# Optimization experiments

Measured on AMD Instinct MI355X. Metric: run time of the kernel, lower is better.

## Reference

```python
import jax, jax.numpy as jnp
import numpy as np
from jax import lax

B, L = 2, 5000            # images, candidate lines per image
C_IN, C_LOI = 256, 128    # backbone channels, dim_loi
H = W = 256               # feature-map spatial size (indices clamped to 255)
N_PTS0, N_PTS1 = 32, 8    # points sampled per line, after maxpool
POOL = N_PTS0 // N_PTS1   # MaxPool1d kernel/stride = 4
PLANES = C_LOI // 2       # Bottleneck1D mid channels
EPS = 1e-5


def setup_inputs() -> dict:
    key = jax.random.key(0)
    ks = jax.random.split(key, 16)
    f32 = jnp.float32
    s = 0.05
    feature = jax.random.normal(ks[0], (B, C_IN, H, W), f32)
    lines = jax.random.uniform(ks[1], (B, L, 2, 2), f32, minval=0.0, maxval=255.0)
    return {
        "feature": feature,
        "lines": lines,
        "fc1_w": jax.random.normal(ks[2], (C_LOI, C_IN), f32) * s,
        "fc1_b": jnp.zeros((C_LOI,), f32),
        "bn1_g": jnp.ones((C_LOI,), f32),
        "bn1_b": jnp.zeros((C_LOI,), f32),
        "bn1_m": jax.random.normal(ks[3], (C_LOI,), f32) * 0.1,
        "bn1_v": jax.random.uniform(ks[4], (C_LOI,), f32, minval=0.5, maxval=1.5),
        "conv1_w": jax.random.normal(ks[5], (PLANES, C_LOI), f32) * s,
        "conv1_b": jnp.zeros((PLANES,), f32),
        "bn2_g": jnp.ones((PLANES,), f32),
        "bn2_b": jnp.zeros((PLANES,), f32),
        "bn2_m": jax.random.normal(ks[6], (PLANES,), f32) * 0.1,
        "bn2_v": jax.random.uniform(ks[7], (PLANES,), f32, minval=0.5, maxval=1.5),
        "conv2_w": jax.random.normal(ks[8], (PLANES, PLANES, 3), f32) * s,
        "conv2_b": jnp.zeros((PLANES,), f32),
        "bn3_g": jnp.ones((PLANES,), f32),
        "bn3_b": jnp.zeros((PLANES,), f32),
        "bn3_m": jax.random.normal(ks[9], (PLANES,), f32) * 0.1,
        "bn3_v": jax.random.uniform(ks[10], (PLANES,), f32, minval=0.5, maxval=1.5),
        "conv3_w": jax.random.normal(ks[11], (C_LOI, PLANES), f32) * s,
        "conv3_b": jnp.zeros((C_LOI,), f32),
        "fc2_w": jax.random.normal(ks[12], (3, C_LOI * N_PTS1), f32) * s,
        "fc2_b": jnp.zeros((3,), f32),
    }


def _bn(x, g, b, m, v):
    # eval-mode BatchNorm1d over [N, C, T]
    inv = g / jnp.sqrt(v + EPS)
    return x * inv[None, :, None] + (b - m * inv)[None, :, None]


def _bilinear_sample(feat, lines):
    # feat: [B, C, H, W], lines: [B, L, 2, 2] -> [B, L, C, N_PTS0]
    lam = jnp.linspace(0.0, 1.0, N_PTS0, dtype=feat.dtype)[:, None]  # [P,1]
    # p = lam * endpoint0 + (1-lam) * endpoint1 - 0.5  -> [B, L, P, 2]
    p = lines[:, :, 0:1, :] * lam + lines[:, :, 1:2, :] * (1.0 - lam) - 0.5
    px, py = p[..., 0], p[..., 1]                       # [B, L, P]
    px0 = jnp.clip(jnp.floor(px), 0.0, 255.0)
    py0 = jnp.clip(jnp.floor(py), 0.0, 255.0)
    px1 = jnp.clip(px0 + 1.0, 0.0, 255.0)
    py1 = jnp.clip(py0 + 1.0, 0.0, 255.0)
    ix0, iy0 = px0.astype(jnp.int32), py0.astype(jnp.int32)
    ix1, iy1 = px1.astype(jnp.int32), py1.astype(jnp.int32)
    w00 = (px1 - px) * (py1 - py)
    w10 = (px - px0) * (py1 - py)
    w01 = (px1 - px) * (py - py0)
    w11 = (px - px0) * (py - py0)

    def one_image(f, a0, b0, a1, b1, c00, c10, c01, c11):
        # f: [C,H,W], indices/weights: [L,P] -> [C,L,P]
        return (f[:, a0, b0] * c00 + f[:, a1, b0] * c10 +
                f[:, a0, b1] * c01 + f[:, a1, b1] * c11)

    xp = jax.vmap(one_image)(feat, ix0, iy0, ix1, iy1, w00, w10, w01, w11)
    return jnp.transpose(xp, (0, 2, 1, 3))  # [B, L, C, P]


def _forward(feature, lines, fc1_w, fc1_b, bn1_g, bn1_b, bn1_m, bn1_v,
             conv1_w, conv1_b, bn2_g, bn2_b, bn2_m, bn2_v,
             conv2_w, conv2_b, bn3_g, bn3_b, bn3_m, bn3_v,
             conv3_w, conv3_b, fc2_w, fc2_b):
    # fc1: 1x1 conv over the backbone feature map
    x = jnp.einsum('oc,bchw->bohw', fc1_w, feature) + fc1_b[None, :, None, None]
    xp = _bilinear_sample(x, lines)                     # [B, L, C_LOI, P]
    xp = xp.reshape(B * L, C_LOI, N_PTS0)
    # MaxPool1d(kernel=POOL, stride=POOL)
    xp = xp.reshape(B * L, C_LOI, N_PTS1, POOL).max(axis=-1)  # [N, C, T]
    # Bottleneck1D residual branch: BN-ReLU-Conv1(k1)-BN-ReLU-Conv(k3)-BN-ReLU-Conv(k1)
    h = jax.nn.relu(_bn(xp, bn1_g, bn1_b, bn1_m, bn1_v))
    h = jnp.einsum('oc,nct->not', conv1_w, h) + conv1_b[None, :, None]
    h = jax.nn.relu(_bn(h, bn2_g, bn2_b, bn2_m, bn2_v))
    h = lax.conv_general_dilated(h, conv2_w, window_strides=(1,),
                                 padding=((1, 1),),
                                 dimension_numbers=('NCH', 'OIH', 'NCH'))
    h = h + conv2_b[None, :, None]
    h = jax.nn.relu(_bn(h, bn3_g, bn3_b, bn3_m, bn3_v))
    h = jnp.einsum('oc,nct->not', conv3_w, h) + conv3_b[None, :, None]
    xp = xp + h
    # fc2: ReLU + Linear(dim_loi * n_pts1 -> 3)
    flat = jax.nn.relu(xp).reshape(B * L, C_LOI * N_PTS1)
    return flat @ fc2_w.T + fc2_b


def reference(feature, lines, fc1_w, fc1_b, bn1_g, bn1_b, bn1_m, bn1_v,
              conv1_w, conv1_b, bn2_g, bn2_b, bn2_m, bn2_v,
              conv2_w, conv2_b, bn3_g, bn3_b, bn3_m, bn3_v,
              conv3_w, conv3_b, fc2_w, fc2_b):
    return _forward(feature, lines, fc1_w, fc1_b, bn1_g, bn1_b, bn1_m, bn1_v,
                    conv1_w, conv1_b, bn2_g, bn2_b, bn2_m, bn2_v,
                    conv2_w, conv2_b, bn3_g, bn3_b, bn3_m, bn3_v,
                    conv3_w, conv3_b, fc2_w, fc2_b)
```

## Files before the change

kernel.cpp:

```cpp
#include <hip/hip_runtime.h>
#include <hip/hip_bf16.h>

#define BB 2
#define LL 5000
#define CIN 256
#define CLOI 128
#define HH 256
#define WW 256
#define HWP (HH*WW)
#define NPTS0 32
#define NPTS1 8
#define PLANES 64
#define EPSV 1e-5f

#define X_BYTES   ((size_t)BB * HWP * CLOI * 2)
#define XS_BYTES  ((size_t)BB * LL * 1024 * 2)
#define W1S_OFF   (X_BYTES + XS_BYTES)
#define W2S_OFF   (W1S_OFF + 16384)
#define W3S_OFF   (W2S_OFF + 24576)
#define B1P_OFF   (W3S_OFF + 16384)
#define B2P_OFF   (B1P_OFF + 256)
#define S1_OFF    (B2P_OFF + 256)
#define T1_OFF    (S1_OFF + 512)
#define W0S_OFF   (T1_OFF + 512)

typedef unsigned int uint;
typedef unsigned short ushort;
typedef __attribute__((ext_vector_type(8))) short short8;
typedef __attribute__((ext_vector_type(4))) float f32x4;

__device__ __forceinline__ float bf2f(ushort u) {
    uint v = ((uint)u) << 16;
    return __uint_as_float(v);
}
__device__ __forceinline__ ushort f2bf(float f) {
    uint x = __float_as_uint(f);
    uint r = (x + 0x7fffu + ((x >> 16) & 1u)) >> 16;
    return (ushort)r;
}
__device__ __forceinline__ uint pack2(float a, float b) {
    return (uint)f2bf(a) | ((uint)f2bf(b) << 16);
}

__global__ __launch_bounds__(256) void fc1_kernel(
    const float* __restrict__ feature, const ushort* __restrict__ w0s,
    const float* __restrict__ fc1_b, ushort* __restrict__ xout)
{
    __shared__ ushort sF[32 * 64 * 8];

    int tid = threadIdx.x;
    int tile = blockIdx.x;
    int b = tile >> 10;
    int p0 = (tile & 1023) << 6;
    int wv = tid >> 6, lane = tid & 63;
    int q = lane >> 4, ln = lane & 15;

    short8 afr[8][2];
#pragma unroll
    for (int kg = 0; kg < 8; kg++)
#pragma unroll
        for (int mt = 0; mt < 2; mt++)
            afr[kg][mt] = *(const short8*)(w0s + ((size_t)((kg * 4 + q) * 128 + wv * 32 + mt * 16 + ln)) * 8);

    const float* fb = feature + (size_t)b * CIN * HWP + p0;
    int g_ = tid >> 4;
    int qd = tid & 15;
#pragma unroll
    for (int s = 0; s < 2; s++) {
        int g = s * 16 + g_;
        const float* src = fb + (size_t)(g * 8) * HWP + qd * 4;
        float4 rv[8];
#pragma unroll
        for (int j = 0; j < 8; j++) rv[j] = *(const float4*)(src + (size_t)j * HWP);
#pragma unroll
        for (int i = 0; i < 4; i++) {
            uint4 u;
            u.x = pack2(((const float*)&rv[0])[i], ((const float*)&rv[1])[i]);
            u.y = pack2(((const float*)&rv[2])[i], ((const float*)&rv[3])[i]);
            u.z = pack2(((const float*)&rv[4])[i], ((const float*)&rv[5])[i]);
            u.w = pack2(((const float*)&rv[6])[i], ((const float*)&rv[7])[i]);
            *(uint4*)(&sF[(g * 64 + qd * 4 + i) * 8]) = u;
        }
    }
    __syncthreads();

    const f32x4 fzero = { 0.f, 0.f, 0.f, 0.f };
    f32x4 acc[2][4];
#pragma unroll
    for (int mt = 0; mt < 2; mt++)
#pragma unroll
        for (int nt = 0; nt < 4; nt++) acc[mt][nt] = fzero;

#pragma unroll
    for (int kg = 0; kg < 8; kg++) {
#pragma unroll
        for (int nt = 0; nt < 4; nt++) {
            short8 bfr = *(short8*)(&sF[((kg * 4 + q) * 64 + nt * 16 + ln) * 8]);
            acc[0][nt] = __builtin_amdgcn_mfma_f32_16x16x32_bf16(afr[kg][0], bfr, acc[0][nt], 0, 0, 0);
            acc[1][nt] = __builtin_amdgcn_mfma_f32_16x16x32_bf16(afr[kg][1], bfr, acc[1][nt], 0, 0, 0);
        }
    }

    float bias[8];
    *(float4*)bias       = *(const float4*)(fc1_b + wv * 32 + q * 4);
    *(float4*)(bias + 4) = *(const float4*)(fc1_b + wv * 32 + 16 + q * 4);
    ushort* xrow = xout + (size_t)b * HWP * CLOI;
#pragma unroll
    for (int mt = 0; mt < 2; mt++)
#pragma unroll
        for (int nt = 0; nt < 4; nt++) {
            uint2 u;
            u.x = pack2(acc[mt][nt][0] + bias[mt * 4 + 0], acc[mt][nt][1] + bias[mt * 4 + 1]);
            u.y = pack2(acc[mt][nt][2] + bias[mt * 4 + 2], acc[mt][nt][3] + bias[mt * 4 + 3]);
            *(uint2*)(xrow + (size_t)(p0 + nt * 16 + ln) * CLOI + wv * 32 + mt * 16 + q * 4) = u;
        }
}

__global__ __launch_bounds__(256) void prep_kernel(
    const float* __restrict__ conv1_w, const float* __restrict__ conv1_b,
    const float* __restrict__ bn2_g, const float* __restrict__ bn2_b,
    const float* __restrict__ bn2_m, const float* __restrict__ bn2_v,
    const float* __restrict__ conv2_w, const float* __restrict__ conv2_b,
    const float* __restrict__ bn3_g, const float* __restrict__ bn3_b,
    const float* __restrict__ bn3_m, const float* __restrict__ bn3_v,
    const float* __restrict__ conv3_w,
    const float* __restrict__ bn1_g, const float* __restrict__ bn1_b,
    const float* __restrict__ bn1_m, const float* __restrict__ bn1_v,
    const float* __restrict__ fc1_w,
    ushort* __restrict__ w1s, ushort* __restrict__ w2s, ushort* __restrict__ w3s,
    float* __restrict__ b1p, float* __restrict__ b2p,
    float* __restrict__ s1o, float* __restrict__ t1o,
    ushort* __restrict__ w0s)
{
    int idx = blockIdx.x * 256 + threadIdx.x;
    if (idx < 8192) {
        int kg = idx >> 9, rem = idx & 511, m = rem >> 3, j = rem & 7;
        int c = kg * 8 + j;
        float s2 = bn2_g[m] * rsqrtf(bn2_v[m] + EPSV);
        w1s[idx] = f2bf(conv1_w[m * 128 + c] * s2);
    }
    if (idx < 12288) {
        int dt = idx >> 12, rem = idx & 4095;
        int kg = rem >> 9, m = (rem >> 3) & 63, j = rem & 7;
        int i = kg * 8 + j;
        float s3 = bn3_g[m] * rsqrtf(bn3_v[m] + EPSV);
        w2s[idx] = f2bf(conv2_w[m * 192 + i * 3 + dt] * s3);
    }
    if (idx < 8192) {
        int kg = idx >> 10, rem = idx & 1023, m = rem >> 3, j = rem & 7;
        w3s[idx] = f2bf(conv3_w[m * 64 + kg * 8 + j]);
    }
    if (idx < 32768) {
        int grp = idx >> 10, rem = idx & 1023, m = rem >> 3, j = rem & 7;
        w0s[idx] = f2bf(fc1_w[m * CIN + grp * 8 + j]);
    }
    if (idx < 64) {
        float s2 = bn2_g[idx] * rsqrtf(bn2_v[idx] + EPSV);
        b1p[idx] = conv1_b[idx] * s2 + bn2_b[idx] - bn2_m[idx] * s2;
        float s3 = bn3_g[idx] * rsqrtf(bn3_v[idx] + EPSV);
        b2p[idx] = conv2_b[idx] * s3 + bn3_b[idx] - bn3_m[idx] * s3;
    }
    if (idx < 128) {
        float s1 = bn1_g[idx] * rsqrtf(bn1_v[idx] + EPSV);
        s1o[idx] = s1;
        t1o[idx] = bn1_b[idx] - bn1_m[idx] * s1;
    }
}

__global__ __launch_bounds__(256, 3) void sample_head_kernel(
    const ushort* __restrict__ x, const float* __restrict__ lines,
    const ushort* __restrict__ w1s, const ushort* __restrict__ w2s,
    const ushort* __restrict__ w3s,
    const float* __restrict__ b1p, const float* __restrict__ b2p,
    const float* __restrict__ s1g, const float* __restrict__ t1g,
    const float* __restrict__ conv3_b,
    const float* __restrict__ fc2_w, const float* __restrict__ fc2_b,
    float* __restrict__ out)
{
    __shared__ ushort sXS[8192];
    __shared__ ushort sH1[8192];
    __shared__ ushort sB2[4096];
    __shared__ int   sIdx[8][32][4];
    __shared__ float sWt[8][32][4];
    __shared__ float sB1[64], sB2b[64], sB3b[128];

    int tid = threadIdx.x;
    int wv = tid >> 6, lane = tid & 63;
    int q = lane >> 4, ln = lane & 15;
    int L0 = blockIdx.x * 8;
    int b = L0 / LL;
    int colg = wv * 16 + ln;

    if (tid < 128) sB3b[tid] = conv3_b[tid];
    if (tid < 64)  { sB1[tid] = b1p[tid]; sB2b[tid] = b2p[tid]; }

    float s1a = s1g[2 * lane], s1c = s1g[2 * lane + 1];
    float t1a = t1g[2 * lane], t1c = t1g[2 * lane + 1];

    {
        int l = tid >> 5, j = tid & 31;
        float lam = (float)j * (1.0f / 31.0f);
        const float* lp = lines + (size_t)(L0 + l) * 4;
        float e0x = lp[0], e0y = lp[1], e1x = lp[2], e1y = lp[3];
        float px = e0x * lam + e1x * (1.f - lam) - 0.5f;
        float py = e0y * lam + e1y * (1.f - lam) - 0.5f;
        float px0 = fminf(fmaxf(floorf(px), 0.f), 255.f);
        float py0 = fminf(fmaxf(floorf(py), 0.f), 255.f);
        float px1 = fminf(px0 + 1.f, 255.f);
        float py1 = fminf(py0 + 1.f, 255.f);
        int ix0 = (int)px0, iy0 = (int)py0, ix1 = (int)px1, iy1 = (int)py1;
        sIdx[l][j][0] = ix0 * WW + iy0;
        sIdx[l][j][1] = ix1 * WW + iy0;
        sIdx[l][j][2] = ix0 * WW + iy1;
        sIdx[l][j][3] = ix1 * WW + iy1;
        sWt[l][j][0] = (px1 - px) * (py1 - py);
        sWt[l][j][1] = (px - px0) * (py1 - py);
        sWt[l][j][2] = (px1 - px) * (py - py0);
        sWt[l][j][3] = (px - px0) * (py - py0);
    }
    __syncthreads();

    const uint* xb = (const uint*)(x + (size_t)b * HWP * CLOI);
    int kg = lane >> 2;
    int j2 = (lane & 3) * 2;
    int swz = (kg & 7) << 3;

    for (int l = 0; l < 8; l++) {
        float m00 = -INFINITY, m10 = -INFINITY;
        float m01 = -INFINITY, m11 = -INFINITY;
#pragma unroll
        for (int jj = 0; jj < 8; jj++) {
            int j = wv * 8 + jj;
            int i00 = sIdx[l][j][0], i10 = sIdx[l][j][1], i01 = sIdx[l][j][2], i11 = sIdx[l][j][3];
            float w00 = sWt[l][j][0], w10 = sWt[l][j][1], w01 = sWt[l][j][2], w11 = sWt[l][j][3];
            uint u00 = xb[(size_t)i00 * 64 + lane];
            uint u10 = xb[(size_t)i10 * 64 + lane];
            uint u01 = xb[(size_t)i01 * 64 + lane];
            uint u11 = xb[(size_t)i11 * 64 + lane];
            float v0 = bf2f((ushort)(u00 & 0xffff)) * w00 + bf2f((ushort)(u10 & 0xffff)) * w10
                     + bf2f((ushort)(u01 & 0xffff)) * w01 + bf2f((ushort)(u11 & 0xffff)) * w11;
            float v1 = bf2f((ushort)(u00 >> 16)) * w00 + bf2f((ushort)(u10 >> 16)) * w10
                     + bf2f((ushort)(u01 >> 16)) * w01 + bf2f((ushort)(u11 >> 16)) * w11;
            if (jj < 4) { m00 = fmaxf(m00, v0); m10 = fmaxf(m10, v1); }
            else        { m01 = fmaxf(m01, v0); m11 = fmaxf(m11, v1); }
        }
        int col0 = l * 8 + 2 * wv;
        int base0 = (kg * 64 + col0) * 8 + j2;
        *(uint*)(&sXS[base0 ^ swz])       = pack2(m00, m10);
        *(uint*)(&sXS[(base0 + 8) ^ swz]) = pack2(m01, m11);
        float h00 = fmaxf(m00 * s1a + t1a, 0.f), h10 = fmaxf(m10 * s1c + t1c, 0.f);
        float h01 = fmaxf(m01 * s1a + t1a, 0.f), h11 = fmaxf(m11 * s1c + t1c, 0.f);
        *(uint*)(&sH1[base0 ^ swz])       = pack2(h00, h10);
        *(uint*)(&sH1[(base0 + 8) ^ swz]) = pack2(h01, h11);
    }
    __syncthreads();

    const short8 bzero = { 0, 0, 0, 0, 0, 0, 0, 0 };
    const f32x4 fzero = { 0.f, 0.f, 0.f, 0.f };

    f32x4 acc1[4];
#pragma unroll
    for (int mt = 0; mt < 4; mt++) acc1[mt] = fzero;
#pragma unroll
    for (int ks = 0; ks < 4; ks++) {
        int kk = ks * 4 + q;
        short8 bfrag = *(short8*)(&sH1[((kk * 64 + colg) * 8) ^ ((kk & 7) << 3)]);
#pragma unroll
        for (int mt = 0; mt < 4; mt++) {
            short8 a = *(const short8*)(w1s + (kk * 64 + mt * 16 + ln) * 8);
            acc1[mt] = __builtin_amdgcn_mfma_f32_16x16x32_bf16(a, bfrag, acc1[mt], 0, 0, 0);
        }
    }
#pragma unroll
    for (int mt = 0; mt < 4; mt++) {
        int m0 = mt * 16 + q * 4;
        float v0 = fmaxf(acc1[mt][0] + sB1[m0 + 0], 0.f);
        float v1 = fmaxf(acc1[mt][1] + sB1[m0 + 1], 0.f);
        float v2 = fmaxf(acc1[mt][2] + sB1[m0 + 2], 0.f);
        float v3 = fmaxf(acc1[mt][3] + sB1[m0 + 3], 0.f);
        uint2 u; u.x = pack2(v0, v1); u.y = pack2(v2, v3);
        *(uint2*)(&sB2[((m0 >> 3) * 64 + colg) * 8 + (m0 & 7)]) = u;
    }
    __syncthreads();

    f32x4 acc2[4];
#pragma unroll
    for (int mt = 0; mt < 4; mt++) acc2[mt] = fzero;
    int tpos = colg & 7;
#pragma unroll
    for (int dt = 0; dt < 3; dt++) {
        int tsh = tpos + dt - 1;
        bool valid = ((unsigned)tsh < 8u);
        int colr = colg + dt - 1;
        colr = colr < 0 ? 0 : (colr > 63 ? 63 : colr);
#pragma unroll
        for (int ks = 0; ks < 2; ks++) {
            int kk = ks * 4 + q;
            short8 bfrag = *(short8*)(&sB2[(kk * 64 + colr) * 8]);
            bfrag = valid ? bfrag : bzero;
#pragma unroll
            for (int mt = 0; mt < 4; mt++) {
                short8 a = *(const short8*)(w2s + dt * 4096 + (kk * 64 + mt * 16 + ln) * 8);
                acc2[mt] = __builtin_amdgcn_mfma_f32_16x16x32_bf16(a, bfrag, acc2[mt], 0, 0, 0);
            }
        }
    }
#pragma unroll
    for (int mt = 0; mt < 4; mt++) {
        int m0 = mt * 16 + q * 4;
        float v0 = fmaxf(acc2[mt][0] + sB2b[m0 + 0], 0.f);
        float v1 = fmaxf(acc2[mt][1] + sB2b[m0 + 1], 0.f);
        float v2 = fmaxf(acc2[mt][2] + sB2b[m0 + 2], 0.f);
        float v3 = fmaxf(acc2[mt][3] + sB2b[m0 + 3], 0.f);
        uint2 u; u.x = pack2(v0, v1); u.y = pack2(v2, v3);
        int idx = ((m0 >> 3) * 64 + colg) * 8 + (m0 & 7);
        *(uint2*)(&sH1[idx ^ (((m0 >> 3) & 7) << 3)]) = u;
    }
    __syncthreads();

    f32x4 acc3[8];
#pragma unroll
    for (int mt = 0; mt < 8; mt++) acc3[mt] = fzero;
#pragma unroll
    for (int ks = 0; ks < 2; ks++) {
        int kk = ks * 4 + q;
        short8 bfrag = *(short8*)(&sH1[((kk * 64 + colg) * 8) ^ ((kk & 7) << 3)]);
#pragma unroll
        for (int mt = 0; mt < 8; mt++) {
            short8 a = *(const short8*)(w3s + (kk * 128 + mt * 16 + ln) * 8);
            acc3[mt] = __builtin_amdgcn_mfma_f32_16x16x32_bf16(a, bfrag, acc3[mt], 0, 0, 0);
        }
    }

    float p0 = 0.f, p1 = 0.f, p2 = 0.f;
#pragma unroll
    for (int mt = 0; mt < 8; mt++) {
#pragma unroll
        for (int r = 0; r < 4; r++) {
            int m = mt * 16 + q * 4 + r;
            int idx = ((m >> 3) * 512 + colg * 8 + (m & 7)) ^ (((m >> 3) & 7) << 3);
            float xsv = bf2f(sXS[idx]);
            float v = fmaxf(xsv + acc3[mt][r] + sB3b[m], 0.f);
            int fi = m * 8 + tpos;
            p0 += v * fc2_w[fi];
            p1 += v * fc2_w[1024 + fi];
            p2 += v * fc2_w[2048 + fi];
        }
    }
    p0 += __shfl_xor(p0, 32); p1 += __shfl_xor(p1, 32); p2 += __shfl_xor(p2, 32);
    p0 += __shfl_xor(p0, 16); p1 += __shfl_xor(p1, 16); p2 += __shfl_xor(p2, 16);
    p0 += __shfl_xor(p0, 4);  p1 += __shfl_xor(p1, 4);  p2 += __shfl_xor(p2, 4);
    p0 += __shfl_xor(p0, 2);  p1 += __shfl_xor(p1, 2);  p2 += __shfl_xor(p2, 2);
    p0 += __shfl_xor(p0, 1);  p1 += __shfl_xor(p1, 1);  p2 += __shfl_xor(p2, 1);

    if (lane == 0 || lane == 8) {
        int line = L0 + wv * 2 + (lane >> 3);
        out[(size_t)line * 3 + 0] = p0 + fc2_b[0];
        out[(size_t)line * 3 + 1] = p1 + fc2_b[1];
        out[(size_t)line * 3 + 2] = p2 + fc2_b[2];
    }
}

extern "C" void kernel_launch(void* const* d_in, const int* in_sizes, int n_in,
                              void* d_out, int out_size, void* d_ws, size_t ws_size,
                              hipStream_t stream) {
    const float* feature = (const float*)d_in[0];
    const float* lines   = (const float*)d_in[1];
    const float* fc1_w   = (const float*)d_in[2];
    const float* fc1_b   = (const float*)d_in[3];
    const float* bn1_g   = (const float*)d_in[4];
    const float* bn1_b   = (const float*)d_in[5];
    const float* bn1_m   = (const float*)d_in[6];
    const float* bn1_v   = (const float*)d_in[7];
    const float* conv1_w = (const float*)d_in[8];
    const float* conv1_b = (const float*)d_in[9];
    const float* bn2_g   = (const float*)d_in[10];
    const float* bn2_b   = (const float*)d_in[11];
    const float* bn2_m   = (const float*)d_in[12];
    const float* bn2_v   = (const float*)d_in[13];
    const float* conv2_w = (const float*)d_in[14];
    const float* conv2_b = (const float*)d_in[15];
    const float* bn3_g   = (const float*)d_in[16];
    const float* bn3_b   = (const float*)d_in[17];
    const float* bn3_m   = (const float*)d_in[18];
    const float* bn3_v   = (const float*)d_in[19];
    const float* conv3_w = (const float*)d_in[20];
    const float* conv3_b = (const float*)d_in[21];
    const float* fc2_w   = (const float*)d_in[22];
    const float* fc2_b   = (const float*)d_in[23];
    float* out = (float*)d_out;

    char* ws = (char*)d_ws;
    ushort* x_bf = (ushort*)ws;
    ushort* w1s  = (ushort*)(ws + W1S_OFF);
    ushort* w2s  = (ushort*)(ws + W2S_OFF);
    ushort* w3s  = (ushort*)(ws + W3S_OFF);
    float*  b1p  = (float*)(ws + B1P_OFF);
    float*  b2p  = (float*)(ws + B2P_OFF);
    float*  s1g  = (float*)(ws + S1_OFF);
    float*  t1g  = (float*)(ws + T1_OFF);
    ushort* w0s  = (ushort*)(ws + W0S_OFF);

    prep_kernel<<<128, 256, 0, stream>>>(
        conv1_w, conv1_b, bn2_g, bn2_b, bn2_m, bn2_v,
        conv2_w, conv2_b, bn3_g, bn3_b, bn3_m, bn3_v,
        conv3_w, bn1_g, bn1_b, bn1_m, bn1_v, fc1_w,
        w1s, w2s, w3s, b1p, b2p, s1g, t1g, w0s);
    fc1_kernel<<<2048, 256, 0, stream>>>(feature, w0s, fc1_b, x_bf);
    sample_head_kernel<<<BB * LL / 8, 256, 0, stream>>>(
        x_bf, lines, w1s, w2s, w3s, b1p, b2p, s1g, t1g, conv3_b, fc2_w, fc2_b, out);
}
```

Measured before the change: 291.8 us.

## Drop sXS shared buffer, keep residual in registers, raise occupancy to 4 blocks

Removes the 16KB sXS shared-memory buffer by holding the pooled residual values in registers (xsu) and later writing them into sH1 once sH1 is free. The conv2 B-fragments are preloaded into registers so sB2 can be reused for the conv2 output. Launch bounds go from 3 to 4 blocks per CU. Index and weight loads from shared memory become int4/float4 vector loads. The aim is less LDS use per block for higher occupancy, which helps hide the latency of the gather-heavy sampling. The cost is more register pressure under a tighter register cap, with a risk of spilling.

```diff
diff --git a/kernel.cpp b/kernel.cpp
--- a/kernel.cpp
+++ b/kernel.cpp
@@ -167,7 +167,7 @@
     }
 }
 
-__global__ __launch_bounds__(256, 3) void sample_head_kernel(
+__global__ __launch_bounds__(256, 4) void sample_head_kernel(
     const ushort* __restrict__ x, const float* __restrict__ lines,
     const ushort* __restrict__ w1s, const ushort* __restrict__ w2s,
     const ushort* __restrict__ w3s,
@@ -177,7 +177,6 @@
     const float* __restrict__ fc2_w, const float* __restrict__ fc2_b,
     float* __restrict__ out)
 {
-    __shared__ ushort sXS[8192];
     __shared__ ushort sH1[8192];
     __shared__ ushort sB2[4096];
     __shared__ int   sIdx[8][32][4];
@@ -225,29 +224,31 @@
     int j2 = (lane & 3) * 2;
     int swz = (kg & 7) << 3;
 
+    uint xsu[8][2];
+#pragma unroll
     for (int l = 0; l < 8; l++) {
         float m00 = -INFINITY, m10 = -INFINITY;
         float m01 = -INFINITY, m11 = -INFINITY;
 #pragma unroll
         for (int jj = 0; jj < 8; jj++) {
             int j = wv * 8 + jj;
-            int i00 = sIdx[l][j][0], i10 = sIdx[l][j][1], i01 = sIdx[l][j][2], i11 = sIdx[l][j][3];
-            float w00 = sWt[l][j][0], w10 = sWt[l][j][1], w01 = sWt[l][j][2], w11 = sWt[l][j][3];
-            uint u00 = xb[(size_t)i00 * 64 + lane];
-            uint u10 = xb[(size_t)i10 * 64 + lane];
-            uint u01 = xb[(size_t)i01 * 64 + lane];
-            uint u11 = xb[(size_t)i11 * 64 + lane];
-            float v0 = bf2f((ushort)(u00 & 0xffff)) * w00 + bf2f((ushort)(u10 & 0xffff)) * w10
-                     + bf2f((ushort)(u01 & 0xffff)) * w01 + bf2f((ushort)(u11 & 0xffff)) * w11;
-            float v1 = bf2f((ushort)(u00 >> 16)) * w00 + bf2f((ushort)(u10 >> 16)) * w10
-                     + bf2f((ushort)(u01 >> 16)) * w01 + bf2f((ushort)(u11 >> 16)) * w11;
+            int4   iv = *(const int4*)(&sIdx[l][j][0]);
+            float4 wvv = *(const float4*)(&sWt[l][j][0]);
+            uint u00 = xb[(size_t)iv.x * 64 + lane];
+            uint u10 = xb[(size_t)iv.y * 64 + lane];
+            uint u01 = xb[(size_t)iv.z * 64 + lane];
+            uint u11 = xb[(size_t)iv.w * 64 + lane];
+            float v0 = bf2f((ushort)(u00 & 0xffff)) * wvv.x + bf2f((ushort)(u10 & 0xffff)) * wvv.y
+                     + bf2f((ushort)(u01 & 0xffff)) * wvv.z + bf2f((ushort)(u11 & 0xffff)) * wvv.w;
+            float v1 = bf2f((ushort)(u00 >> 16)) * wvv.x + bf2f((ushort)(u10 >> 16)) * wvv.y
+                     + bf2f((ushort)(u01 >> 16)) * wvv.z + bf2f((ushort)(u11 >> 16)) * wvv.w;
             if (jj < 4) { m00 = fmaxf(m00, v0); m10 = fmaxf(m10, v1); }
             else        { m01 = fmaxf(m01, v0); m11 = fmaxf(m11, v1); }
         }
+        xsu[l][0] = pack2(m00, m10);
+        xsu[l][1] = pack2(m01, m11);
         int col0 = l * 8 + 2 * wv;
         int base0 = (kg * 64 + col0) * 8 + j2;
-        *(uint*)(&sXS[base0 ^ swz])       = pack2(m00, m10);
-        *(uint*)(&sXS[(base0 + 8) ^ swz]) = pack2(m01, m11);
         float h00 = fmaxf(m00 * s1a + t1a, 0.f), h10 = fmaxf(m10 * s1c + t1c, 0.f);
         float h01 = fmaxf(m01 * s1a + t1a, 0.f), h11 = fmaxf(m11 * s1c + t1c, 0.f);
         *(uint*)(&sH1[base0 ^ swz])       = pack2(h00, h10);
@@ -283,10 +284,16 @@
     }
     __syncthreads();
 
-    f32x4 acc2[4];
-#pragma unroll
-    for (int mt = 0; mt < 4; mt++) acc2[mt] = fzero;
+#pragma unroll
+    for (int l = 0; l < 8; l++) {
+        int col0 = l * 8 + 2 * wv;
+        int base0 = (kg * 64 + col0) * 8 + j2;
+        *(uint*)(&sH1[base0 ^ swz])       = xsu[l][0];
+        *(uint*)(&sH1[(base0 + 8) ^ swz]) = xsu[l][1];
+    }
+
     int tpos = colg & 7;
+    short8 bfr2[3][2];
 #pragma unroll
     for (int dt = 0; dt < 3; dt++) {
         int tsh = tpos + dt - 1;
@@ -295,16 +302,26 @@
         colr = colr < 0 ? 0 : (colr > 63 ? 63 : colr);
 #pragma unroll
         for (int ks = 0; ks < 2; ks++) {
+            short8 bfrag = *(short8*)(&sB2[((ks * 4 + q) * 64 + colr) * 8]);
+            bfr2[dt][ks] = valid ? bfrag : bzero;
+        }
+    }
+    __syncthreads();
+
+    f32x4 acc2[4];
+#pragma unroll
+    for (int mt = 0; mt < 4; mt++) acc2[mt] = fzero;
+#pragma unroll
+    for (int dt = 0; dt < 3; dt++)
+#pragma unroll
+        for (int ks = 0; ks < 2; ks++) {
             int kk = ks * 4 + q;
-            short8 bfrag = *(short8*)(&sB2[(kk * 64 + colr) * 8]);
-            bfrag = valid ? bfrag : bzero;
 #pragma unroll
             for (int mt = 0; mt < 4; mt++) {
                 short8 a = *(const short8*)(w2s + dt * 4096 + (kk * 64 + mt * 16 + ln) * 8);
-                acc2[mt] = __builtin_amdgcn_mfma_f32_16x16x32_bf16(a, bfrag, acc2[mt], 0, 0, 0);
+                acc2[mt] = __builtin_amdgcn_mfma_f32_16x16x32_bf16(a, bfr2[dt][ks], acc2[mt], 0, 0, 0);
             }
         }
-    }
 #pragma unroll
     for (int mt = 0; mt < 4; mt++) {
         int m0 = mt * 16 + q * 4;
@@ -313,8 +330,7 @@
         float v2 = fmaxf(acc2[mt][2] + sB2b[m0 + 2], 0.f);
         float v3 = fmaxf(acc2[mt][3] + sB2b[m0 + 3], 0.f);
         uint2 u; u.x = pack2(v0, v1); u.y = pack2(v2, v3);
-        int idx = ((m0 >> 3) * 64 + colg) * 8 + (m0 & 7);
-        *(uint2*)(&sH1[idx ^ (((m0 >> 3) & 7) << 3)]) = u;
+        *(uint2*)(&sB2[((m0 >> 3) * 64 + colg) * 8 + (m0 & 7)]) = u;
     }
     __syncthreads();
 
@@ -324,7 +340,7 @@
 #pragma unroll
     for (int ks = 0; ks < 2; ks++) {
         int kk = ks * 4 + q;
-        short8 bfrag = *(short8*)(&sH1[((kk * 64 + colg) * 8) ^ ((kk & 7) << 3)]);
+        short8 bfrag = *(short8*)(&sB2[(kk * 64 + colg) * 8]);
 #pragma unroll
         for (int mt = 0; mt < 8; mt++) {
             short8 a = *(const short8*)(w3s + (kk * 128 + mt * 16 + ln) * 8);
@@ -339,7 +355,7 @@
         for (int r = 0; r < 4; r++) {
             int m = mt * 16 + q * 4 + r;
             int idx = ((m >> 3) * 512 + colg * 8 + (m & 7)) ^ (((m >> 3) & 7) << 3);
-            float xsv = bf2f(sXS[idx]);
+            float xsv = bf2f(sH1[idx]);
             float v = fmaxf(xsv + acc3[mt][r] + sB3b[m], 0.f);
             int fi = m * 8 + tpos;
             p0 += v * fc2_w[fi];
```

After: 298.3 us. +2.2%, slower.
